# Performance work log

Measured on AMD Instinct MI355X. Metric: run time of the kernel, lower is better.

## Reference

```python
import jax, jax.numpy as jnp
import numpy as np

N_QUBITS = 8
INPUT_DIM = 256
SEQ_LEN = 256
BATCH = 512


def qgate(theta, x):
    # Closed-form expectation of the PennyLane circuit:
    #   RX(x_i) then RY(theta_i) on each wire (from |0>), then CNOT chain 0->1->...->n-1,
    #   measure <Z_k>.  Single-wire <Z_j> = cos(x_j) * cos(theta_j); CNOT chain maps
    #   Z_k -> Z_0 Z_1 ... Z_k in the Heisenberg picture, so on the product state
    #   <Z_k> = prod_{j<=k} cos(x_j) cos(theta_j).
    # x: (B, n_wires), theta: (n_wires,)
    return jnp.cumprod(jnp.cos(x) * jnp.cos(theta), axis=-1)


def setup_inputs() -> dict:
    key = jax.random.key(0)
    ks = jax.random.split(key, 14)
    d_in = INPUT_DIM + N_QUBITS  # concat([x, hx]) -> 264
    lin_scale = 1.0 / np.sqrt(d_in)
    inp = {
        "inputs": jax.random.normal(ks[0], (SEQ_LEN, BATCH, INPUT_DIM), dtype=jnp.float32),
        "Wf": jax.random.normal(ks[1], (N_QUBITS, d_in), dtype=jnp.float32) * lin_scale,
        "bf": jax.random.normal(ks[2], (N_QUBITS,), dtype=jnp.float32) * lin_scale,
        "Wi": jax.random.normal(ks[3], (N_QUBITS, d_in), dtype=jnp.float32) * lin_scale,
        "bi": jax.random.normal(ks[4], (N_QUBITS,), dtype=jnp.float32) * lin_scale,
        "Wu": jax.random.normal(ks[5], (N_QUBITS, d_in), dtype=jnp.float32) * lin_scale,
        "bu": jax.random.normal(ks[6], (N_QUBITS,), dtype=jnp.float32) * lin_scale,
        "Wo": jax.random.normal(ks[7], (N_QUBITS, d_in), dtype=jnp.float32) * lin_scale,
        "bo": jax.random.normal(ks[8], (N_QUBITS,), dtype=jnp.float32) * lin_scale,
        "pf": jax.random.normal(ks[9], (N_QUBITS,), dtype=jnp.float32),
        "pi_": jax.random.normal(ks[10], (N_QUBITS,), dtype=jnp.float32),
        "pu": jax.random.normal(ks[11], (N_QUBITS,), dtype=jnp.float32),
        "po": jax.random.normal(ks[12], (N_QUBITS,), dtype=jnp.float32),
    }
    return inp


def reference(inputs, Wf, bf, Wi, bi, Wu, bu, Wo, bo, pf, pi_, pu, po):
    B = inputs.shape[1]
    H = pf.shape[0]  # hidden_dim == n_qubits

    def step(carry, x):
        hx, cx = carry
        comb = jnp.concatenate([x, hx], axis=1)  # (B, input_dim + H)
        f = jax.nn.sigmoid(qgate(pf, comb @ Wf.T + bf))
        i = jax.nn.sigmoid(qgate(pi_, comb @ Wi.T + bi))
        g = jnp.tanh(qgate(pu, comb @ Wu.T + bu))
        o = jax.nn.sigmoid(qgate(po, comb @ Wo.T + bo))
        cx = f * cx + i * g
        hx = o * jnp.tanh(cx)
        return (hx, cx), hx

    init = (jnp.zeros((B, H), dtype=inputs.dtype), jnp.zeros((B, H), dtype=inputs.dtype))
    (hx, cx), stacked = jax.lax.scan(step, init, inputs)
    return stacked, hx, cx
```

## Files before the change

kernel.cpp:

```cpp
#include <hip/hip_runtime.h>
#include <hip/hip_bf16.h>


#define SEQ   256
#define BATCH 512
#define DIN   256
#define NROWS (SEQ * BATCH)
#define DCOMB 264
#define MCHUNKS 4

typedef __attribute__((ext_vector_type(8))) short short8;
typedef __attribute__((ext_vector_type(4))) float f32x4;
typedef __attribute__((ext_vector_type(2))) float f32x2;

__device__ __forceinline__ short f2bf(float f) {
    union { __hip_bfloat16 h; short s; } u;
    u.h = __float2bfloat16(f);
    return u.s;
}
__device__ __forceinline__ float bf2f(short s) {
    union { short s; __hip_bfloat16 h; } u;
    u.s = s;
    return __bfloat162float(u.h);
}

__device__ __forceinline__ short8 pack8(float4 a, float4 b) {
    union { short8 s8; int i[4]; } u;
    union { __hip_bfloat162 h; int i; } v;
    v.h = __float22bfloat162_rn(make_float2(a.x, a.y)); u.i[0] = v.i;
    v.h = __float22bfloat162_rn(make_float2(a.z, a.w)); u.i[1] = v.i;
    v.h = __float22bfloat162_rn(make_float2(b.x, b.y)); u.i[2] = v.i;
    v.h = __float22bfloat162_rn(make_float2(b.z, b.w)); u.i[3] = v.i;
    return u.s8;
}

__global__ __launch_bounds__(256) void qlstm_gemm(
    const float* __restrict__ X,
    const float* __restrict__ Wf, const float* __restrict__ Wi,
    const float* __restrict__ Wu, const float* __restrict__ Wo,
    const float* __restrict__ bfv, const float* __restrict__ biv,
    const float* __restrict__ buv, const float* __restrict__ bov,
    float* __restrict__ Z)
{
    const int l   = threadIdx.x & 63;
    const int wid = threadIdx.x >> 6;
    const int lm  = l & 15;
    const int lk  = l >> 4;

    const float* Wg[4] = {Wf, Wi, Wu, Wo};
    const float* Bg[4] = {bfv, biv, buv, bov};

    short8 Bhi[2][8], Blo[2][8];
    float bias[2];
    #pragma unroll
    for (int nt = 0; nt < 2; ++nt) {
        const int c = nt * 16 + lm;
        const float* wrow = Wg[c & 3] + (c >> 2) * DCOMB;
        bias[nt] = Bg[c & 3][c >> 2];
        #pragma unroll
        for (int ks = 0; ks < 8; ++ks) {
            const float* p = wrow + ks * 32 + lk * 8;
            const float4 w0 = *(const float4*)p;
            const float4 w1 = *(const float4*)(p + 4);
            const float wv[8] = {w0.x, w0.y, w0.z, w0.w, w1.x, w1.y, w1.z, w1.w};
            #pragma unroll
            for (int j = 0; j < 8; ++j) {
                const short hi = f2bf(wv[j]);
                Bhi[nt][ks][j] = hi;
                Blo[nt][ks][j] = f2bf(wv[j] - bf2f(hi));
            }
        }
    }

    #pragma unroll
    for (int ch = 0; ch < MCHUNKS; ++ch) {
        const int row0 = (blockIdx.x * MCHUNKS + ch) * 64 + wid * 16;
        const float* xbase = X + (long)(row0 + lm) * DIN + lk * 8;

        float4 xv[16];
        #pragma unroll
        for (int i = 0; i < 16; ++i)
            xv[i] = *(const float4*)(xbase + (i >> 1) * 32 + (i & 1) * 4);

        f32x4 acc0 = (f32x4){bias[0], bias[0], bias[0], bias[0]};
        f32x4 acc1 = (f32x4){bias[1], bias[1], bias[1], bias[1]};
        #pragma unroll
        for (int ks = 0; ks < 8; ++ks) {
            const short8 a = pack8(xv[2 * ks], xv[2 * ks + 1]);
            acc0 = __builtin_amdgcn_mfma_f32_16x16x32_bf16(a, Bhi[0][ks], acc0, 0, 0, 0);
            acc0 = __builtin_amdgcn_mfma_f32_16x16x32_bf16(a, Blo[0][ks], acc0, 0, 0, 0);
            acc1 = __builtin_amdgcn_mfma_f32_16x16x32_bf16(a, Bhi[1][ks], acc1, 0, 0, 0);
            acc1 = __builtin_amdgcn_mfma_f32_16x16x32_bf16(a, Blo[1][ks], acc1, 0, 0, 0);
        }

        #pragma unroll
        for (int r = 0; r < 4; ++r) {
            Z[(long)(row0 + lk * 4 + r) * 32 + lm]      = acc0[r];
            Z[(long)(row0 + lk * 4 + r) * 32 + 16 + lm] = acc1[r];
        }
    }
}

#define DPP_ROR(V, S) \
    __int_as_float(__builtin_amdgcn_update_dpp(__float_as_int(V), __float_as_int(V), 0x120 | (S), 0xF, 0xF, false))
#define SWAP8(V) \
    __int_as_float(__builtin_amdgcn_update_dpp(__float_as_int(V), __float_as_int(V), 0x128, 0xF, 0xF, false))
#define DPP_REPL8(V) \
    __int_as_float(__builtin_amdgcn_update_dpp(__float_as_int(V), __float_as_int(V), 0x118, 0xF, 0xF, false))

#define PSTG(A, D, PM) { \
    float s0_ = __int_as_float(__builtin_amdgcn_update_dpp(one_i, __float_as_int(A.x), 0x110 | (D), 0xF, 0xF, false)); \
    float s1_ = __int_as_float(__builtin_amdgcn_update_dpp(one_i, __float_as_int(A.y), 0x110 | (D), 0xF, 0xF, false)); \
    A *= (f32x2){ (PM) ? s0_ : 1.0f, (PM) ? s1_ : 1.0f }; }

#define PF 8

__global__ __launch_bounds__(64, 1) void qlstm_scan(
    const float* __restrict__ Z,
    const float* __restrict__ Wf, const float* __restrict__ Wi,
    const float* __restrict__ Wu, const float* __restrict__ Wo,
    const float* __restrict__ pf, const float* __restrict__ pi_,
    const float* __restrict__ pu, const float* __restrict__ po,
    float* __restrict__ out)
{
    const int tx  = threadIdx.x;
    const int q   = tx & 15;
    const int kq  = q & 7;
    const int hi  = q >> 3;
    const int b   = (blockIdx.x * 64 + tx) >> 4;
    const int oidx = b * 8 + kq;
    const int woff = kq * DCOMB + DIN;

    const float* WgA = hi ? Wu : Wf;
    const float* WgB = hi ? Wo : Wi;
    f32x2 wp[8];
    #pragma unroll
    for (int s = 0; s < 8; ++s) {
        const int j = (kq - s) & 7;
        wp[s] = (f32x2){WgA[woff + j], WgB[woff + j]};
    }
    const f32x2 cth = (f32x2){__cosf((hi ? pu : pf)[kq]),
                              __cosf((hi ? po : pi_)[kq])};

    const float SK1 = 0.25f, SK2 = -0.0208333333f, SK3 = 0.0020833333f,
                SK4 = -0.00021082f;
    const f32x2 k0 = (f32x2){hi ? 0.0f : 0.5f, 0.5f};
    const f32x2 k1 = (f32x2){hi ? 0.9999016f : SK1, SK1};
    const f32x2 k2 = (f32x2){hi ? -0.3310485f : SK2, SK2};
    const f32x2 k3 = (f32x2){hi ? 0.1204423f : SK3, SK3};
    const f32x2 k4 = (f32x2){hi ? -0.0277012f : SK4, SK4};

    const bool pm1 = kq >= 1, pm2 = kq >= 2, pm4 = kq >= 4;
    const int one_i = __float_as_int(1.0f);

    float hx = 0.0f, cx = 0.0f;
    const float2* __restrict__ Zv2 = (const float2*)Z;
    const int zoff = b * 16 + kq * 2 + hi;
    float* __restrict__ outp = out + oidx;

    float2 ring[PF];
    #pragma unroll
    for (int i = 0; i < PF; ++i) ring[i] = Zv2[(i << 13) + zoff];

    for (int t0 = 0; t0 < SEQ; t0 += PF) {
        #pragma unroll
        for (int u = 0; u < PF; ++u) {
            const int t = t0 + u;
            const float2 z2 = ring[u];
            int tn = t + PF; if (tn > SEQ - 1) tn = SEQ - 1;
            ring[u] = Zv2[(tn << 13) + zoff];

            const float h0 = hx;
            const float h1 = DPP_ROR(hx, 1), h2 = DPP_ROR(hx, 2);
            const float h3 = DPP_ROR(hx, 3), h4 = DPP_ROR(hx, 4);
            const float h5 = DPP_ROR(hx, 5), h6 = DPP_ROR(hx, 6);
            const float h7 = DPP_ROR(hx, 7);

            f32x2 ca = (f32x2){h0, h0} * wp[0] + (f32x2){h1, h1} * wp[1];
            f32x2 cb = (f32x2){h4, h4} * wp[4] + (f32x2){h5, h5} * wp[5];
            ca += (f32x2){h2, h2} * wp[2];
            cb += (f32x2){h6, h6} * wp[6];
            ca += (f32x2){h3, h3} * wp[3];
            cb += (f32x2){h7, h7} * wp[7];
            const f32x2 p = ((f32x2){z2.x, z2.y} + ca) + cb;

            f32x2 A = (f32x2){__cosf(p.x), __cosf(p.y)} * cth;
            PSTG(A, 1, pm1) PSTG(A, 2, pm2) PSTG(A, 4, pm4)

            const f32x2 t2 = A * A;
            f32x2 r = k3 + t2 * k4;
            r = k2 + t2 * r;
            r = k1 + t2 * r;
            const f32x2 P = k0 + A * r;
            const float v1 = P.x;
            const float v2 = P.y;

            const float swu = SWAP8(v1);
            cx = fmaf(v1, cx, v2 * swu);

            const float tq  = cx * cx;
            const float num = cx * fmaf(tq, fmaf(tq, 1.0f, 105.0f), 945.0f);
            const float den = fmaf(tq, fmaf(tq, 15.0f, 420.0f), 945.0f);
            const float tc  = num * __builtin_amdgcn_rcpf(den);

            const float stc = SWAP8(tc);
            const float hh  = v2 * stc;
            hx = SWAP8(hh);
            hx = DPP_REPL8(hx);

            outp[t << 12] = hx;
        }
    }
    if (q < 8) {
        out[NROWS * 8 + oidx]        = hx;
        out[NROWS * 8 + 4096 + oidx] = cx;
    }
}

extern "C" void kernel_launch(void* const* d_in, const int* in_sizes, int n_in,
                              void* d_out, int out_size, void* d_ws, size_t ws_size,
                              hipStream_t stream) {
    const float* X   = (const float*)d_in[0];
    const float* Wf  = (const float*)d_in[1];
    const float* bfv = (const float*)d_in[2];
    const float* Wi  = (const float*)d_in[3];
    const float* biv = (const float*)d_in[4];
    const float* Wu  = (const float*)d_in[5];
    const float* buv = (const float*)d_in[6];
    const float* Wo  = (const float*)d_in[7];
    const float* bov = (const float*)d_in[8];
    const float* pf  = (const float*)d_in[9];
    const float* pi_ = (const float*)d_in[10];
    const float* pu  = (const float*)d_in[11];
    const float* po  = (const float*)d_in[12];
    float* out = (float*)d_out;
    float* Z   = (float*)d_ws;

    qlstm_gemm<<<NROWS / (64 * MCHUNKS), 256, 0, stream>>>(
        X, Wf, Wi, Wu, Wo, bfv, biv, buv, bov, Z);
    qlstm_scan<<<128, 64, 0, stream>>>(Z, Wf, Wi, Wu, Wo, pf, pi_, pu, po, out);
}
```

Measured before the change: 267.2 us.

## Interleave gate lanes so quad-perm DPP replaces swap/broadcast chain in recurrence

```diff
diff --git a/kernel.cpp b/kernel.cpp
--- a/kernel.cpp
+++ b/kernel.cpp
@@ -103,15 +103,13 @@
 
 #define DPP_ROR(V, S) \
     __int_as_float(__builtin_amdgcn_update_dpp(__float_as_int(V), __float_as_int(V), 0x120 | (S), 0xF, 0xF, false))
-#define SWAP8(V) \
-    __int_as_float(__builtin_amdgcn_update_dpp(__float_as_int(V), __float_as_int(V), 0x128, 0xF, 0xF, false))
-#define DPP_REPL8(V) \
-    __int_as_float(__builtin_amdgcn_update_dpp(__float_as_int(V), __float_as_int(V), 0x118, 0xF, 0xF, false))
-
-#define PSTG(A, D, PM) { \
+#define QP(V, CTRL) \
+    __int_as_float(__builtin_amdgcn_update_dpp(__float_as_int(V), __float_as_int(V), (CTRL), 0xF, 0xF, false))
+
+#define PSTG2(A, D) { \
     float s0_ = __int_as_float(__builtin_amdgcn_update_dpp(one_i, __float_as_int(A.x), 0x110 | (D), 0xF, 0xF, false)); \
     float s1_ = __int_as_float(__builtin_amdgcn_update_dpp(one_i, __float_as_int(A.y), 0x110 | (D), 0xF, 0xF, false)); \
-    A *= (f32x2){ (PM) ? s0_ : 1.0f, (PM) ? s1_ : 1.0f }; }
+    A *= (f32x2){s0_, s1_}; }
 
 #define PF 8
 
@@ -125,8 +123,8 @@
 {
     const int tx  = threadIdx.x;
     const int q   = tx & 15;
-    const int kq  = q & 7;
-    const int hi  = q >> 3;
+    const int kq  = q >> 1;
+    const int hi  = q & 1;
     const int b   = (blockIdx.x * 64 + tx) >> 4;
     const int oidx = b * 8 + kq;
     const int woff = kq * DCOMB + DIN;
@@ -150,12 +148,11 @@
     const f32x2 k3 = (f32x2){hi ? 0.1204423f : SK3, SK3};
     const f32x2 k4 = (f32x2){hi ? -0.0277012f : SK4, SK4};
 
-    const bool pm1 = kq >= 1, pm2 = kq >= 2, pm4 = kq >= 4;
     const int one_i = __float_as_int(1.0f);
 
     float hx = 0.0f, cx = 0.0f;
     const float2* __restrict__ Zv2 = (const float2*)Z;
-    const int zoff = b * 16 + kq * 2 + hi;
+    const int zoff = b * 16 + q;
     float* __restrict__ outp = out + oidx;
 
     float2 ring[PF];
@@ -171,47 +168,44 @@
             ring[u] = Zv2[(tn << 13) + zoff];
 
             const float h0 = hx;
-            const float h1 = DPP_ROR(hx, 1), h2 = DPP_ROR(hx, 2);
-            const float h3 = DPP_ROR(hx, 3), h4 = DPP_ROR(hx, 4);
-            const float h5 = DPP_ROR(hx, 5), h6 = DPP_ROR(hx, 6);
-            const float h7 = DPP_ROR(hx, 7);
-
-            f32x2 ca = (f32x2){h0, h0} * wp[0] + (f32x2){h1, h1} * wp[1];
-            f32x2 cb = (f32x2){h4, h4} * wp[4] + (f32x2){h5, h5} * wp[5];
-            ca += (f32x2){h2, h2} * wp[2];
-            cb += (f32x2){h6, h6} * wp[6];
-            ca += (f32x2){h3, h3} * wp[3];
-            cb += (f32x2){h7, h7} * wp[7];
-            const f32x2 p = ((f32x2){z2.x, z2.y} + ca) + cb;
+            const float h1 = DPP_ROR(hx, 2),  h2 = DPP_ROR(hx, 4);
+            const float h3 = DPP_ROR(hx, 6),  h4 = DPP_ROR(hx, 8);
+            const float h5 = DPP_ROR(hx, 10), h6 = DPP_ROR(hx, 12);
+            const float h7 = DPP_ROR(hx, 14);
+
+            f32x2 e0 = (f32x2){h0, h0} * wp[0] + (f32x2){h1, h1} * wp[1];
+            f32x2 e1 = (f32x2){h2, h2} * wp[2] + (f32x2){h3, h3} * wp[3];
+            f32x2 e2 = (f32x2){h4, h4} * wp[4] + (f32x2){h5, h5} * wp[5];
+            f32x2 e3 = (f32x2){h6, h6} * wp[6] + (f32x2){h7, h7} * wp[7];
+            const f32x2 p = (((f32x2){z2.x, z2.y} + e0) + (e1 + e2)) + e3;
 
             f32x2 A = (f32x2){__cosf(p.x), __cosf(p.y)} * cth;
-            PSTG(A, 1, pm1) PSTG(A, 2, pm2) PSTG(A, 4, pm4)
+            PSTG2(A, 2) PSTG2(A, 4) PSTG2(A, 8)
 
             const f32x2 t2 = A * A;
             f32x2 r = k3 + t2 * k4;
             r = k2 + t2 * r;
             r = k1 + t2 * r;
             const f32x2 P = k0 + A * r;
-            const float v1 = P.x;
-            const float v2 = P.y;
-
-            const float swu = SWAP8(v1);
-            cx = fmaf(v1, cx, v2 * swu);
+
+            const float f_all = QP(P.x, 0xA0);
+            const float u_all = QP(P.x, 0xF5);
+            const float i_all = QP(P.y, 0xA0);
+            const float o_all = QP(P.y, 0xF5);
+
+            cx = fmaf(f_all, cx, i_all * u_all);
 
             const float tq  = cx * cx;
             const float num = cx * fmaf(tq, fmaf(tq, 1.0f, 105.0f), 945.0f);
             const float den = fmaf(tq, fmaf(tq, 15.0f, 420.0f), 945.0f);
             const float tc  = num * __builtin_amdgcn_rcpf(den);
 
-            const float stc = SWAP8(tc);
-            const float hh  = v2 * stc;
-            hx = SWAP8(hh);
-            hx = DPP_REPL8(hx);
+            hx = o_all * tc;
 
             outp[t << 12] = hx;
         }
     }
-    if (q < 8) {
+    if (hi == 0) {
         out[NROWS * 8 + oidx]        = hx;
         out[NROWS * 8 + 4096 + oidx] = cx;
     }
```

Measured after the change: 262.5 us. No clear change (-1.7%).
